# Kernel tuning notes

Hardware: AMD Instinct MI355X
Metric: run time of the kernel (lower is better)

The kernel has to match this reference:

```python
import jax, jax.numpy as jnp
import numpy as np

QLEN, MLEN, CMLEN, BSZ, D_MODEL = 1024, 1024, 512, 2, 1024
N_HEAD, D_HEAD, D_INNER = 16, 64, 4096
KLEN = MLEN + CMLEN + QLEN
LN_EPS = 1e-5


def _layer_norm(x, scale, bias):
    mu = jnp.mean(x, axis=-1, keepdims=True)
    var = jnp.var(x, axis=-1, keepdims=True)
    return (x - mu) * jax.lax.rsqrt(var + LN_EPS) * scale + bias


def _rel_shift(x):
    # x: [qlen, klen, bsz, n_head]  (Transformer-XL relative shift)
    q, k, b, n = x.shape
    x = jnp.concatenate([jnp.zeros((q, 1, b, n), x.dtype), x], axis=1)
    x = x.reshape(k + 1, q, b, n)[1:]
    return x.reshape(q, k, b, n)


def setup_inputs() -> dict:
    key = jax.random.key(0)
    ks = jax.random.split(key, 10)
    s = 0.02
    # causal mask: query i (absolute pos MLEN_TOT+i) cannot attend to key j > MLEN_TOT+i
    mlen_tot = KLEN - QLEN
    i = jnp.arange(QLEN)[:, None]
    j = jnp.arange(KLEN)[None, :]
    attn_mask = j > (i + mlen_tot)
    return {
        "input_ids": jax.random.normal(ks[0], (QLEN, BSZ, D_MODEL), jnp.float32),
        "pos_emb": jax.random.normal(ks[1], (KLEN, D_MODEL), jnp.float32),
        "mem": jax.random.normal(ks[2], (MLEN, BSZ, D_MODEL), jnp.float32),
        "c_mem": jax.random.normal(ks[3], (CMLEN, BSZ, D_MODEL), jnp.float32),
        "attn_mask": attn_mask,
        "qkv_w": jax.random.normal(ks[4], (D_MODEL, 3 * N_HEAD * D_HEAD), jnp.float32) * s,
        "r_w": jax.random.normal(ks[5], (D_MODEL, N_HEAD * D_HEAD), jnp.float32) * s,
        "o_w": jax.random.normal(ks[6], (N_HEAD * D_HEAD, D_MODEL), jnp.float32) * s,
        "r_w_bias": jax.random.normal(ks[7], (N_HEAD, D_HEAD), jnp.float32) * s,
        "r_r_bias": jax.random.normal(ks[8], (N_HEAD, D_HEAD), jnp.float32) * s,
        "ln_attn_scale": jnp.ones((D_MODEL,), jnp.float32),
        "ln_attn_bias": jnp.zeros((D_MODEL,), jnp.float32),
        "ff_w1": jax.random.normal(ks[9], (D_MODEL, D_INNER), jnp.float32) * s,
        "ff_b1": jnp.zeros((D_INNER,), jnp.float32),
        "ff_w2": jax.random.normal(jax.random.fold_in(key, 11), (D_INNER, D_MODEL), jnp.float32) * s,
        "ff_b2": jnp.zeros((D_MODEL,), jnp.float32),
        "ln_ff_scale": jnp.ones((D_MODEL,), jnp.float32),
        "ln_ff_bias": jnp.zeros((D_MODEL,), jnp.float32),
    }


def reference(input_ids, pos_emb, mem, c_mem, attn_mask, qkv_w, r_w, o_w,
              r_w_bias, r_r_bias, ln_attn_scale, ln_attn_bias,
              ff_w1, ff_b1, ff_w2, ff_b2, ln_ff_scale, ln_ff_bias):
    qlen, bsz, d_model = input_ids.shape
    n_head, d_head = r_w_bias.shape
    scale = 1.0 / np.sqrt(d_head)

    # _concat_memories + cat with current sequence (seq-first, dim 0)
    mems = jnp.concatenate([mem, c_mem], axis=0)
    cat = jnp.concatenate([mems, input_ids], axis=0)          # [klen, b, d]

    w_heads = cat @ qkv_w                                     # [klen, b, 3*h*dh]
    w_q, w_k, w_v = jnp.split(w_heads, 3, axis=-1)
    w_q = w_q[-qlen:]
    klen = w_k.shape[0]

    w_q = w_q.reshape(qlen, bsz, n_head, d_head)
    w_k = w_k.reshape(klen, bsz, n_head, d_head)
    w_v = w_v.reshape(klen, bsz, n_head, d_head)
    r_k = (pos_emb @ r_w).reshape(klen, n_head, d_head)       # [klen, h, dh]

    AC = jnp.einsum('ibnd,jbnd->ijbn', w_q + r_w_bias, w_k)
    BD = jnp.einsum('ibnd,jnd->ijbn', w_q + r_r_bias, r_k)
    BD = _rel_shift(BD)
    attn_score = (AC + BD) * scale                            # [q, k, b, h]

    attn_score = jnp.where(attn_mask[:, :, None, None], jnp.float32(-1e30), attn_score)
    attn_prob = jax.nn.softmax(attn_score, axis=1)

    attn_vec = jnp.einsum('ijbn,jbnd->ibnd', attn_prob, w_v)
    attn_vec = attn_vec.reshape(qlen, bsz, n_head * d_head)
    attn_out = attn_vec @ o_w

    # post-lnorm residual (pre_lnorm=False)
    attn_res = _layer_norm(input_ids + attn_out, ln_attn_scale, ln_attn_bias)

    # PositionwiseFF (post-lnorm)
    h = jax.nn.relu(attn_res @ ff_w1 + ff_b1) @ ff_w2 + ff_b2
    out = _layer_norm(attn_res + h, ln_ff_scale, ln_ff_bias)
    return out
```

## Files before the change

kernel.cpp:

```cpp
#include <hip/hip_runtime.h>
#include <hip/hip_bf16.h>

#define QLEN 1024
#define KLEN 2560
#define MTOT 1536
#define BSZ 2
#define NH 16
#define DH 64
#define DMODEL 1024
#define DINNER 4096

typedef short bf16x8 __attribute__((ext_vector_type(8)));
typedef float f32x4  __attribute__((ext_vector_type(4)));

__device__ __forceinline__ short f2bf(float f) {
    union { float f; unsigned u; } v; v.f = f;
    unsigned r = v.u + 0x7FFFu + ((v.u >> 16) & 1u);
    return (short)(r >> 16);
}
__device__ __forceinline__ float bf2f(short s) {
    union { unsigned u; float f; } v; v.u = ((unsigned)(unsigned short)s) << 16;
    return v.f;
}
__device__ __forceinline__ unsigned pack2(float a, float b) {
    unsigned pk;
    asm("v_cvt_pk_bf16_f32 %0, %1, %2" : "=v"(pk) : "v"(a), "v"(b));
    return pk;
}

#define GLOAD16(g, l)                                                        \
    __builtin_amdgcn_global_load_lds(                                        \
        (const __attribute__((address_space(1))) unsigned int*)(g),          \
        (__attribute__((address_space(3))) unsigned int*)(l), 16, 0, 0)

__device__ __forceinline__ void tr_body(
    const float* __restrict__ in, short* __restrict__ out,
    int K, int N, int bx, int by, int tid, float (*ts)[65])
{
    const int k0 = by * 64, n0 = bx * 64;
    const int r = tid >> 2, cb = (tid & 3) * 16;
    #pragma unroll
    for (int u = 0; u < 16; u += 4) {
        const float4 v = *(const float4*)(in + (size_t)(k0 + r) * N + n0 + cb + u);
        ts[r][cb + u] = v.x; ts[r][cb + u + 1] = v.y;
        ts[r][cb + u + 2] = v.z; ts[r][cb + u + 3] = v.w;
    }
    __syncthreads();
    #pragma unroll
    for (int p = 0; p < 4; p++) {
        const int wr_ = (tid >> 4) + p * 16;
        const int c   = (tid & 15) * 4;
        uint2 pk;
        pk.x = pack2(ts[c][wr_], ts[c + 1][wr_]);
        pk.y = pack2(ts[c + 2][wr_], ts[c + 3][wr_]);
        *(uint2*)(out + (size_t)(n0 + wr_) * K + k0 + c) = pk;
    }
}

__global__ __launch_bounds__(256) void prep_all(
    const float* __restrict__ mem, const float* __restrict__ cmem,
    const float* __restrict__ inp, short* __restrict__ catb,
    const float* __restrict__ pos, short* __restrict__ posb,
    const float* __restrict__ qkv_w, short* __restrict__ qkv_wt,
    const float* __restrict__ r_w, short* __restrict__ r_wt,
    const float* __restrict__ o_w, short* __restrict__ o_wt,
    const float* __restrict__ ff_w1, short* __restrict__ ff1t,
    const float* __restrict__ ff_w2, short* __restrict__ ff2t)
{
    __shared__ float ts[64][65];
    const int bid = blockIdx.x;
    const int tid = threadIdx.x;
    if (bid < 2560) {
        const int i = bid * 256 + tid;
        const int row = i >> 7, c = (i & 127) * 8;
        const float* src;
        if (row < 2048)      src = mem  + (size_t)row * 1024;
        else if (row < 3072) src = cmem + (size_t)(row - 2048) * 1024;
        else                 src = inp  + (size_t)(row - 3072) * 1024;
        const float4 a = *(const float4*)(src + c);
        const float4 b = *(const float4*)(src + c + 4);
        uint4 o;
        o.x = pack2(a.x, a.y); o.y = pack2(a.z, a.w);
        o.z = pack2(b.x, b.y); o.w = pack2(b.z, b.w);
        *(uint4*)(catb + (size_t)i * 8) = o;
    } else if (bid < 3840) {
        const int i = (bid - 2560) * 256 + tid;
        const float4 a = *(const float4*)(pos + (size_t)i * 8);
        const float4 b = *(const float4*)(pos + (size_t)i * 8 + 4);
        uint4 o;
        o.x = pack2(a.x, a.y); o.y = pack2(a.z, a.w);
        o.z = pack2(b.x, b.y); o.w = pack2(b.z, b.w);
        *(uint4*)(posb + (size_t)i * 8) = o;
    } else if (bid < 4608) {
        const int r = bid - 3840; tr_body(qkv_w, qkv_wt, 1024, 3072, r % 48, r / 48, tid, ts);
    } else if (bid < 4864) {
        const int r = bid - 4608; tr_body(r_w, r_wt, 1024, 1024, r % 16, r / 16, tid, ts);
    } else if (bid < 5120) {
        const int r = bid - 4864; tr_body(o_w, o_wt, 1024, 1024, r % 16, r / 16, tid, ts);
    } else if (bid < 6144) {
        const int r = bid - 5120; tr_body(ff_w1, ff1t, 1024, 4096, r % 64, r / 64, tid, ts);
    } else {
        const int r = bid - 6144; tr_body(ff_w2, ff2t, 4096, 1024, r % 16, r / 16, tid, ts);
    }
}

__global__ __launch_bounds__(256) void vt_conv(
    const short* __restrict__ wh, short* __restrict__ vt)
{
    __shared__ short Ts[64][72];
    const int j0 = blockIdx.x * 64;
    const int bn = blockIdx.y;
    const int b = bn >> 4, n = bn & 15;
    const int tid = threadIdx.x;
    {
        const int key = tid >> 2, c = (tid & 3) * 16;
        const short* p = wh + ((size_t)(j0 + key) * BSZ + b) * 3072 + 2048 + n * 64 + c;
        *(bf16x8*)&Ts[key][c]     = *(const bf16x8*)p;
        *(bf16x8*)&Ts[key][c + 8] = *(const bf16x8*)(p + 8);
    }
    __syncthreads();
    {
        const int d = tid >> 2, kc = (tid & 3) * 16;
        __attribute__((aligned(16))) short tmp[16];
        #pragma unroll
        for (int u = 0; u < 16; u++) tmp[u] = Ts[kc + u][d];
        short* q = vt + ((size_t)(bn * 64) + d) * KLEN + j0 + kc;
        *(uint4*)q       = *(uint4*)tmp;
        *(uint4*)(q + 8) = *((uint4*)tmp + 1);
    }
}

__device__ __forceinline__ void gemm_core(
    const short* __restrict__ A, const short* __restrict__ Bt,
    short* As, short* Bs, int Kfull, int klen, int bm, int bn,
    int tid, f32x4 acc[4][4])
{
    const int w  = tid >> 6;
    const int l  = tid & 63;
    const int lg = l >> 4, lc = l & 15;
    const int wr = w >> 1, wc = w & 1;
    const int srow = 2 * w * 16 + (l >> 2);
    const int scol = (l & 3) * 8;
    const size_t aoff0 = (size_t)(bm + srow) * Kfull + scol;
    const size_t boff0 = (size_t)(bn + srow) * Kfull + scol;
    const size_t rstep = (size_t)16 * Kfull;
    const int ch0 = 2 * w * 512, ch1 = (2 * w + 1) * 512;

    GLOAD16(A + aoff0, As + ch0);
    GLOAD16(A + aoff0 + rstep, As + ch1);
    GLOAD16(Bt + boff0, Bs + ch0);
    GLOAD16(Bt + boff0 + rstep, Bs + ch1);
    __syncthreads();

    int cur = 0;
    for (int k0 = 0; k0 < klen; k0 += 32) {
        const int nb = (cur ^ 1) * 4096;
        if (k0 + 32 < klen) {
            GLOAD16(A + aoff0 + k0 + 32, As + nb + ch0);
            GLOAD16(A + aoff0 + rstep + k0 + 32, As + nb + ch1);
            GLOAD16(Bt + boff0 + k0 + 32, Bs + nb + ch0);
            GLOAD16(Bt + boff0 + rstep + k0 + 32, Bs + nb + ch1);
        }
        const int cb = cur * 4096;
        bf16x8 af[4], bfr[4];
        #pragma unroll
        for (int m = 0; m < 4; m++)
            af[m] = *(const bf16x8*)(As + cb + (wr * 64 + m * 16 + lc) * 32 + lg * 8);
        #pragma unroll
        for (int n = 0; n < 4; n++)
            bfr[n] = *(const bf16x8*)(Bs + cb + (wc * 64 + n * 16 + lc) * 32 + lg * 8);
        #pragma unroll
        for (int m = 0; m < 4; m++)
            #pragma unroll
            for (int n = 0; n < 4; n++)
                acc[m][n] = __builtin_amdgcn_mfma_f32_16x16x32_bf16(
                    af[m], bfr[n], acc[m][n], 0, 0, 0);
        __syncthreads();
        cur ^= 1;
    }
}

__global__ __launch_bounds__(256) void gemm_g12(
    const short* __restrict__ catb, const short* __restrict__ qkv_wt,
    short* __restrict__ whb,
    const short* __restrict__ posb, const short* __restrict__ r_wt,
    short* __restrict__ rkb)
{
    __shared__ short As[8192], Bs[8192];
    const int tid = threadIdx.x;
    const int id0 = blockIdx.x;
    int id = (id0 & 7) * 116 + (id0 >> 3);
    const short *A, *Bt; short* Cb; int N, bm, bn;
    if (id < 384) {
        A = catb; Bt = qkv_wt; Cb = whb; N = 3072;
        bm = (id >> 4) * 128; bn = (8 + (id & 15)) * 128;
    } else if (id < 768) {
        id -= 384;
        A = catb; Bt = qkv_wt; Cb = whb; N = 3072;
        bm = (24 + id / 24) * 128; bn = (id % 24) * 128;
    } else {
        id -= 768;
        A = posb; Bt = r_wt; Cb = rkb; N = 1024;
        bm = (id / 8) * 128; bn = (id % 8) * 128;
    }

    f32x4 acc[4][4];
    #pragma unroll
    for (int m = 0; m < 4; m++)
        #pragma unroll
        for (int n = 0; n < 4; n++) acc[m][n] = (f32x4){0.f, 0.f, 0.f, 0.f};
    gemm_core(A, Bt, As, Bs, 1024, 1024, bm, bn, tid, acc);

    const int w = tid >> 6, l = tid & 63, lg = l >> 4, lc = l & 15;
    const int wr = w >> 1, wc = w & 1;
    #pragma unroll
    for (int m = 0; m < 4; m++)
        #pragma unroll
        for (int n = 0; n < 4; n++) {
            const int col = bn + wc * 64 + n * 16 + lc;
            #pragma unroll
            for (int r = 0; r < 4; r++) {
                const int row = bm + wr * 64 + m * 16 + lg * 4 + r;
                Cb[(size_t)row * N + col] = f2bf(acc[m][n][r]);
            }
        }
}

__global__ __launch_bounds__(256) void gemm_relu(
    const short* __restrict__ A, const short* __restrict__ Bt,
    const float* __restrict__ bias, short* __restrict__ Cb,
    int N, int K)
{
    __shared__ short As[8192], Bs[8192];
    const int tid = threadIdx.x;
    const int nbx = N >> 7;
    const int lid = blockIdx.x;
    const int nwg8 = gridDim.x >> 3;
    const int swz = (lid & 7) * nwg8 + (lid >> 3);
    const int bn = (swz % nbx) * 128, bm = (swz / nbx) * 128;
    f32x4 acc[4][4];
    #pragma unroll
    for (int m = 0; m < 4; m++)
        #pragma unroll
        for (int n = 0; n < 4; n++) acc[m][n] = (f32x4){0.f, 0.f, 0.f, 0.f};
    gemm_core(A, Bt, As, Bs, K, K, bm, bn, tid, acc);

    const int w = tid >> 6, l = tid & 63, lg = l >> 4, lc = l & 15;
    const int wr = w >> 1, wc = w & 1;
    #pragma unroll
    for (int m = 0; m < 4; m++)
        #pragma unroll
        for (int n = 0; n < 4; n++) {
            const int col = bn + wc * 64 + n * 16 + lc;
            const float bv = bias[col];
            #pragma unroll
            for (int r = 0; r < 4; r++) {
                const int row = bm + wr * 64 + m * 16 + lg * 4 + r;
                Cb[(size_t)row * N + col] = f2bf(fmaxf(acc[m][n][r] + bv, 0.0f));
            }
        }
}

__global__ __launch_bounds__(256) void gemm_split(
    const short* __restrict__ A, const short* __restrict__ Bt,
    float* __restrict__ C0, float* __restrict__ C1,
    int N, int Kfull, int Ksub)
{
    __shared__ short As[8192], Bs[8192];
    const int tid = threadIdx.x;
    const int nbx = N >> 7;
    const int lid = blockIdx.x;
    const int nwg8 = gridDim.x >> 3;
    const int swz = (lid & 7) * nwg8 + (lid >> 3);
    const int bn = (swz % nbx) * 128;
    const int rest = swz / nbx;
    const int bm = (rest & 15) * 128;
    const int z = rest >> 4;
    float* C = z ? C1 : C0;
    f32x4 acc[4][4];
    #pragma unroll
    for (int m = 0; m < 4; m++)
        #pragma unroll
        for (int n = 0; n < 4; n++) acc[m][n] = (f32x4){0.f, 0.f, 0.f, 0.f};
    gemm_core(A + z * Ksub, Bt + z * Ksub, As, Bs, Kfull, Ksub, bm, bn, tid, acc);

    const int w = tid >> 6, l = tid & 63, lg = l >> 4, lc = l & 15;
    const int wr = w >> 1, wc = w & 1;
    #pragma unroll
    for (int m = 0; m < 4; m++)
        #pragma unroll
        for (int n = 0; n < 4; n++) {
            const int col = bn + wc * 64 + n * 16 + lc;
            #pragma unroll
            for (int r = 0; r < 4; r++) {
                const int row = bm + wr * 64 + m * 16 + lg * 4 + r;
                C[(size_t)row * N + col] = acc[m][n][r];
            }
        }
}

__global__ __launch_bounds__(512, 2) void attn_mfma(
    const short* __restrict__ wh,
    const short* __restrict__ vt,
    const short* __restrict__ rk,
    const float* __restrict__ rwb,
    const float* __restrict__ rrb,
    short* __restrict__ po,
    float* __restrict__ ml)
{
    __shared__ __align__(16) short Ks[2][64 * 64];
    __shared__ __align__(16) short Vs[2][64 * 64];
    __shared__ __align__(16) short Rs[256 * 64];
    __shared__ __align__(16) short Ps[8][16 * 64];

    const int bid = blockIdx.x;
    const int ibp = (bid >> 3) & 7;
    const int z   = (bid >> 6) & 1;
    const int bn  = ((bid & 7) << 2) | (bid >> 7);
    const int i0  = ibp * 128;
    const int b   = bn >> 4, n = bn & 15;
    const int tid = threadIdx.x;
    const int w   = tid >> 6;
    const int l   = tid & 63;
    const int lg  = l >> 4;
    const int lc  = l & 15;
    const int i_base = i0 + 16 * w;

    bf16x8 aqw[2], aqr[2];
    {
        const int i = i_base + lc;
        const short* qp = wh + ((size_t)(MTOT + i) * BSZ + b) * 3072 + n * 64;
        #pragma unroll
        for (int kc2 = 0; kc2 < 2; kc2++) {
            const bf16x8 q8 = *(const bf16x8*)(qp + kc2 * 32 + lg * 8);
            const int d0 = kc2 * 32 + lg * 8;
            #pragma unroll
            for (int e = 0; e < 8; e++) {
                const float qv = bf2f(q8[e]);
                aqw[kc2][e] = f2bf(qv + rwb[n * 64 + d0 + e]);
                aqr[kc2][e] = f2bf(qv + rrb[n * 64 + d0 + e]);
            }
        }
    }

    f32x4 o_acc[4];
    #pragma unroll
    for (int nt = 0; nt < 4; nt++) o_acc[nt] = (f32x4){0.f, 0.f, 0.f, 0.f};
    float mrun[4]  = {0.f, 0.f, 0.f, 0.f};
    float lpart[4] = {0.f, 0.f, 0.f, 0.f};

    const int jend   = i0 + 1664;
    const int jhalf  = i0 / 2 + 832;
    const int jstart = z ? jhalf : 0;
    const int jstop  = z ? jend  : jhalf;

    const int kr = tid >> 3, kc = tid & 7;
    const size_t whK = (size_t)b * 3072 + 1024 + n * 64;
    const size_t vtK = (size_t)(bn * 64) * KLEN;
    const int mbase0 = jstart - i0 + 896;

    #pragma unroll
    for (int u = 0; u < 3; u++) {
        const int m = mbase0 + kr + 64 * u;
        bf16x8 rv = (bf16x8){0, 0, 0, 0, 0, 0, 0, 0};
        if (m < KLEN)
            rv = *(const bf16x8*)(rk + (size_t)m * 1024 + n * 64 + kc * 8);
        const int slot = m & 255;
        *(bf16x8*)(Rs + slot * 64 + ((kc ^ (slot & 7)) * 8)) = rv;
    }
    {
        const bf16x8 k0 = *(const bf16x8*)(wh + (size_t)(jstart + kr) * (BSZ * 3072) + whK + kc * 8);
        const bf16x8 v0 = *(const bf16x8*)(vt + vtK + (size_t)kr * KLEN + jstart + kc * 8);
        *(bf16x8*)(Ks[0] + kr * 64 + ((kc ^ (kr & 7)) * 8)) = k0;
        *(bf16x8*)(Vs[0] + kr * 64 + ((kc ^ (kr & 7)) * 8)) = v0;
    }
    bf16x8 pk = (bf16x8){0,0,0,0,0,0,0,0}, pv = pk, pr;
    {
        const int jn = jstart + 64;
        if (jn < jstop) {
            pk = *(const bf16x8*)(wh + (size_t)(jn + kr) * (BSZ * 3072) + whK + kc * 8);
            pv = *(const bf16x8*)(vt + vtK + (size_t)kr * KLEN + jn + kc * 8);
        }
        const int m = mbase0 + 192 + kr;
        pr = (m < KLEN) ? *(const bf16x8*)(rk + (size_t)m * 1024 + n * 64 + kc * 8)
                        : (bf16x8){0, 0, 0, 0, 0, 0, 0, 0};
    }

    int cur = 0;
    for (int j0 = jstart; j0 < jstop; j0 += 64) {
        const int mbase = j0 - i0 + 896;
        __syncthreads();
        *(bf16x8*)(Ks[cur ^ 1] + kr * 64 + ((kc ^ (kr & 7)) * 8)) = pk;
        *(bf16x8*)(Vs[cur ^ 1] + kr * 64 + ((kc ^ (kr & 7)) * 8)) = pv;
        {
            const int mw = mbase + 192 + kr;
            const int slot = mw & 255;
            *(bf16x8*)(Rs + slot * 64 + ((kc ^ (slot & 7)) * 8)) = pr;
        }
        {
            const int jn = j0 + 128;
            if (jn < jstop) {
                pk = *(const bf16x8*)(wh + (size_t)(jn + kr) * (BSZ * 3072) + whK + kc * 8);
                pv = *(const bf16x8*)(vt + vtK + (size_t)kr * KLEN + jn + kc * 8);
            }
            const int m = mbase + 256 + kr;
            pr = (m < KLEN) ? *(const bf16x8*)(rk + (size_t)m * 1024 + n * 64 + kc * 8)
                            : (bf16x8){0, 0, 0, 0, 0, 0, 0, 0};
        }

        __builtin_amdgcn_s_setprio(1);
        f32x4 sfr[4];
        #pragma unroll
        for (int jt = 0; jt < 4; jt++) {
            const int row = 16 * jt + lc;
            const int c0 = (lg ^ (row & 7)) * 8, c1 = ((4 + lg) ^ (row & 7)) * 8;
            const bf16x8 bk0 = *(const bf16x8*)(Ks[cur] + row * 64 + c0);
            const bf16x8 bk1 = *(const bf16x8*)(Ks[cur] + row * 64 + c1);
            f32x4 acc = (f32x4){0.f, 0.f, 0.f, 0.f};
            acc = __builtin_amdgcn_mfma_f32_16x16x32_bf16(aqw[0], bk0, acc, 0, 0, 0);
            acc = __builtin_amdgcn_mfma_f32_16x16x32_bf16(aqw[1], bk1, acc, 0, 0, 0);
            sfr[jt] = acc;
        }
        f32x4 dr[5];
        #pragma unroll
        for (int mt = 0; mt < 5; mt++) {
            const int slot = (mbase + 16 * mt + lc + 112 - 16 * w) & 255;
            const int c0 = (lg ^ (slot & 7)) * 8, c1 = ((4 + lg) ^ (slot & 7)) * 8;
            const bf16x8 br0 = *(const bf16x8*)(Rs + slot * 64 + c0);
            const bf16x8 br1 = *(const bf16x8*)(Rs + slot * 64 + c1);
            f32x4 acc = (f32x4){0.f, 0.f, 0.f, 0.f};
            acc = __builtin_amdgcn_mfma_f32_16x16x32_bf16(aqr[0], br0, acc, 0, 0, 0);
            acc = __builtin_amdgcn_mfma_f32_16x16x32_bf16(aqr[1], br1, acc, 0, 0, 0);
            dr[mt] = acc;
        }
        __builtin_amdgcn_s_setprio(0);

        #pragma unroll
        for (int r = 0; r < 4; r++) {
            const int q   = 4 * lg + r;
            const int o   = lc + 15 - q;
            const int src = (l & 48) | (o & 15);
            float sv[4];
            float mx = -1e30f;
            #pragma unroll
            for (int jt = 0; jt < 4; jt++) {
                const float v0 = __shfl(dr[jt][r], src);
                const float v1 = __shfl(dr[jt + 1][r], src);
                const float bd = (o < 16) ? v0 : v1;
                float s = (sfr[jt][r] + bd) * 0.125f;
                if (z) {
                    const int j = j0 + 16 * jt + lc;
                    if (j > i_base + q + MTOT) s = -1e30f;
                }
                sv[jt] = s;
                mx = fmaxf(mx, s);
            }
            if (__any(mx - mrun[r] > 8.0f)) {
                #pragma unroll
                for (int msk = 1; msk <= 8; msk <<= 1)
                    mx = fmaxf(mx, __shfl_xor(mx, msk));
                const float mnew = fmaxf(mrun[r], mx);
                const float corr = __expf(mrun[r] - mnew);
                mrun[r] = mnew;
                lpart[r] *= corr;
                #pragma unroll
                for (int nt = 0; nt < 4; nt++) o_acc[nt][r] *= corr;
            }
            float p0 = __expf(sv[0] - mrun[r]);
            float p1 = __expf(sv[1] - mrun[r]);
            float p2 = __expf(sv[2] - mrun[r]);
            float p3 = __expf(sv[3] - mrun[r]);
            lpart[r] += (p0 + p1) + (p2 + p3);
            const unsigned pk01 = pack2(p0, p1);
            const unsigned pk23 = pack2(p2, p3);
            short* pw = Ps[w] + q * 64 + (lc & 7);
            const int qs = q & 7;
            pw[(((0 + (lc >> 3)) ^ qs) * 8)] = (short)(pk01 & 0xffffu);
            pw[(((2 + (lc >> 3)) ^ qs) * 8)] = (short)(pk01 >> 16);
            pw[(((4 + (lc >> 3)) ^ qs) * 8)] = (short)(pk23 & 0xffffu);
            pw[(((6 + (lc >> 3)) ^ qs) * 8)] = (short)(pk23 >> 16);
        }

        asm volatile("s_waitcnt lgkmcnt(0)" ::: "memory");
        __builtin_amdgcn_sched_barrier(0);

        __builtin_amdgcn_s_setprio(1);
        const int pc0 = (lg ^ (lc & 7)) * 8, pc1 = ((4 + lg) ^ (lc & 7)) * 8;
        const bf16x8 pa0 = *(const bf16x8*)(Ps[w] + lc * 64 + pc0);
        const bf16x8 pa1 = *(const bf16x8*)(Ps[w] + lc * 64 + pc1);
        #pragma unroll
        for (int nt = 0; nt < 4; nt++) {
            const int row = 16 * nt + lc;
            const int c0 = (lg ^ (row & 7)) * 8, c1 = ((4 + lg) ^ (row & 7)) * 8;
            const bf16x8 bv0 = *(const bf16x8*)(Vs[cur] + row * 64 + c0);
            const bf16x8 bv1 = *(const bf16x8*)(Vs[cur] + row * 64 + c1);
            o_acc[nt] = __builtin_amdgcn_mfma_f32_16x16x32_bf16(pa0, bv0, o_acc[nt], 0, 0, 0);
            o_acc[nt] = __builtin_amdgcn_mfma_f32_16x16x32_bf16(pa1, bv1, o_acc[nt], 0, 0, 0);
        }
        __builtin_amdgcn_s_setprio(0);
        cur ^= 1;
    }

    const size_t blk = (size_t)z * 256 + ibp * 32 + bn;
    #pragma unroll
    for (int r = 0; r < 4; r++) {
        float lr = lpart[r];
        #pragma unroll
        for (int msk = 1; msk <= 8; msk <<= 1)
            lr += __shfl_xor(lr, msk);
        const int q = 16 * w + 4 * lg + r;
        #pragma unroll
        for (int nt = 0; nt < 4; nt++)
            po[(blk * 128 + q) * 64 + 16 * nt + lc] = f2bf(o_acc[nt][r]);
        if (lc == 0) {
            ml[(blk * 128 + q) * 2 + 0] = mrun[r];
            ml[(blk * 128 + q) * 2 + 1] = lr;
        }
    }
}

__global__ __launch_bounds__(256) void attn_merge(
    const short* __restrict__ po, const float* __restrict__ ml,
    short* __restrict__ av)
{
    const int blk = blockIdx.x;
    const int ib2 = blk >> 5, bn = blk & 31;
    const int b = bn >> 4, n = bn & 15;
    const int tid = threadIdx.x;
    const int q64 = tid >> 2, dc = (tid & 3) * 16;
    const int i = ib2 * 64 + q64;
    const size_t r0 = ((size_t)(i >> 7) * 32 + bn) * 128 + (i & 127);
    const size_t r1 = ((size_t)(256 + (i >> 7) * 32 + bn)) * 128 + (i & 127);
    const float m0 = ml[r0 * 2], l0 = ml[r0 * 2 + 1];
    const float m1 = ml[r1 * 2], l1 = ml[r1 * 2 + 1];
    const float M = fmaxf(m0, m1);
    const float c0 = __expf(m0 - M), c1 = __expf(m1 - M);
    const float invL = 1.0f / (l0 * c0 + l1 * c1);
    const bf16x8 a0 = *(const bf16x8*)(po + r0 * 64 + dc);
    const bf16x8 a1 = *(const bf16x8*)(po + r0 * 64 + dc + 8);
    const bf16x8 b0 = *(const bf16x8*)(po + r1 * 64 + dc);
    const bf16x8 b1 = *(const bf16x8*)(po + r1 * 64 + dc + 8);
    __attribute__((aligned(16))) short ov[16];
    #pragma unroll
    for (int e = 0; e < 8; e++) {
        ov[e]     = f2bf((bf2f(a0[e]) * c0 + bf2f(b0[e]) * c1) * invL);
        ov[e + 8] = f2bf((bf2f(a1[e]) * c0 + bf2f(b1[e]) * c1) * invL);
    }
    short* op = av + ((size_t)i * BSZ + b) * 1024 + n * 64 + dc;
    *(uint4*)op       = *(uint4*)ov;
    *(uint4*)(op + 8) = *((uint4*)ov + 1);
}

template <bool WB, bool HASB>
__global__ __launch_bounds__(256) void ln_fuse(
    const float* __restrict__ p0, const float* __restrict__ p1,
    const float* __restrict__ badd, const float* __restrict__ res,
    const float* __restrict__ scale, const float* __restrict__ bias,
    float* __restrict__ out, short* __restrict__ outb)
{
    const int row = blockIdx.x;
    const int tid = threadIdx.x;
    const size_t base = (size_t)row * 1024 + tid * 4;
    const float4 a = *(const float4*)(p0 + base);
    const float4 b = *(const float4*)(p1 + base);
    const float4 rv = *(const float4*)(res + base);
    float v[4] = {a.x + b.x + rv.x, a.y + b.y + rv.y,
                  a.z + b.z + rv.z, a.w + b.w + rv.w};
    if (HASB) {
        const float4 bb = *(const float4*)(badd + tid * 4);
        v[0] += bb.x; v[1] += bb.y; v[2] += bb.z; v[3] += bb.w;
    }
    float s  = v[0] + v[1] + v[2] + v[3];
    float ss = v[0]*v[0] + v[1]*v[1] + v[2]*v[2] + v[3]*v[3];
    #pragma unroll
    for (int off = 32; off >= 1; off >>= 1) {
        s  += __shfl_down(s, off);
        ss += __shfl_down(ss, off);
    }
    __shared__ float red[8];
    const int lane = tid & 63, wid = tid >> 6;
    if (lane == 0) { red[wid] = s; red[4 + wid] = ss; }
    __syncthreads();
    if (tid == 0) {
        red[0] = red[0] + red[1] + red[2] + red[3];
        red[4] = red[4] + red[5] + red[6] + red[7];
    }
    __syncthreads();
    const float mean = red[0] * (1.0f / 1024.0f);
    const float var  = red[4] * (1.0f / 1024.0f) - mean * mean;
    const float rstd = rsqrtf(var + 1e-5f);
    const float4 sc = *(const float4*)(scale + tid * 4);
    const float4 bi = *(const float4*)(bias + tid * 4);
    float4 o;
    o.x = (v[0] - mean) * rstd * sc.x + bi.x;
    o.y = (v[1] - mean) * rstd * sc.y + bi.y;
    o.z = (v[2] - mean) * rstd * sc.z + bi.z;
    o.w = (v[3] - mean) * rstd * sc.w + bi.w;
    *(float4*)(out + base) = o;
    if (WB) {
        uint2 pk;
        pk.x = pack2(o.x, o.y);
        pk.y = pack2(o.z, o.w);
        *(uint2*)(outb + base) = pk;
    }
}

extern "C" void kernel_launch(void* const* d_in, const int* in_sizes, int n_in,
                              void* d_out, int out_size, void* d_ws, size_t ws_size,
                              hipStream_t stream) {
    const float* input_ids = (const float*)d_in[0];
    const float* pos_emb   = (const float*)d_in[1];
    const float* mem       = (const float*)d_in[2];
    const float* c_mem     = (const float*)d_in[3];
    const float* qkv_w     = (const float*)d_in[5];
    const float* r_w       = (const float*)d_in[6];
    const float* o_w       = (const float*)d_in[7];
    const float* r_w_bias  = (const float*)d_in[8];
    const float* r_r_bias  = (const float*)d_in[9];
    const float* ln_a_s    = (const float*)d_in[10];
    const float* ln_a_b    = (const float*)d_in[11];
    const float* ff_w1     = (const float*)d_in[12];
    const float* ff_b1     = (const float*)d_in[13];
    const float* ff_w2     = (const float*)d_in[14];
    const float* ff_b2     = (const float*)d_in[15];
    const float* ln_f_s    = (const float*)d_in[16];
    const float* ln_f_b    = (const float*)d_in[17];

    char* base = (char*)d_ws;
    short* o_wt   = (short*)(base + 0);
    short* ff1t   = (short*)(base + 2097152);
    short* ff2t   = (short*)(base + 10485760);
    short* whb    = (short*)(base + 18874368);
    short* rkb    = (short*)(base + 50331648);
    short* qkv_wt = (short*)(base + 55574528);
    short* catb   = (short*)(base + 61865984);
    short* posb   = (short*)(base + 72351744);
    short* r_wt   = (short*)(base + 77594624);
    short* vtb    = (short*)(base + 55574528);
    short* po     = (short*)(base + 66060288);
    float* mlb    = (float*)(base + 74448896);
    short* avb    = (short*)(base + 74973184);
    float* hp0    = (float*)(base + 18874368);
    float* hp1    = (float*)(base + 27262976);
    float* ares   = (float*)(base + 35651584);
    short* aresb  = (short*)(base + 44040192);
    short* h1b    = (short*)(base + 48234496);

    const dim3 thr(256);

    prep_all<<<dim3(7168), thr, 0, stream>>>(
        mem, c_mem, input_ids, catb, pos_emb, posb,
        qkv_w, qkv_wt, r_w, r_wt, o_w, o_wt, ff_w1, ff1t, ff_w2, ff2t);
    gemm_g12<<<dim3(928), thr, 0, stream>>>(catb, qkv_wt, whb, posb, r_wt, rkb);
    vt_conv<<<dim3(40, 32), thr, 0, stream>>>(whb, vtb);
    attn_mfma<<<dim3(512), dim3(512), 0, stream>>>(
        whb, vtb, rkb, r_w_bias, r_r_bias, po, mlb);
    attn_merge<<<dim3(512), thr, 0, stream>>>(po, mlb, avb);
    gemm_split<<<dim3(256), thr, 0, stream>>>(
        avb, o_wt, hp0, hp1, 1024, 1024, 512);
    ln_fuse<true, false><<<dim3(2048), thr, 0, stream>>>(
        hp0, hp1, nullptr, input_ids, ln_a_s, ln_a_b, ares, aresb);
    gemm_relu<<<dim3(512), thr, 0, stream>>>(aresb, ff1t, ff_b1, h1b, 4096, 1024);
    gemm_split<<<dim3(256), thr, 0, stream>>>(
        h1b, ff2t, hp0, hp1, 1024, 4096, 2048);
    ln_fuse<false, true><<<dim3(2048), thr, 0, stream>>>(
        hp0, hp1, ff_b2, ares, ln_f_s, ln_f_b, (float*)d_out, nullptr);
}
```

Before: 249.7 us.

## Triple-buffer GEMM LDS with single barrier and read bf16 residual in final LN

The shared GEMM core moves from double to triple buffering of LDS tiles. Global loads are issued two k-steps ahead, and each iteration uses an explicit vmcnt wait plus one barrier instead of two __syncthreads. Separately, the first layernorm no longer writes an fp32 copy of its output, and the second layernorm reads the bf16 residual instead. This saves memory traffic but introduces an extra bf16 rounding of the residual. LDS per block grows from 32KB to 48KB, which may lower occupancy.

Measured after the change: 263.9 us. +5.7%, slower.

```diff
diff --git a/kernel.cpp b/kernel.cpp
--- a/kernel.cpp
+++ b/kernel.cpp
@@ -150,33 +150,41 @@
     GLOAD16(A + aoff0 + rstep, As + ch1);
     GLOAD16(Bt + boff0, Bs + ch0);
     GLOAD16(Bt + boff0 + rstep, Bs + ch1);
-    __syncthreads();
-
-    int cur = 0;
+    if (32 < klen) {
+        GLOAD16(A + aoff0 + 32, As + 4096 + ch0);
+        GLOAD16(A + aoff0 + rstep + 32, As + 4096 + ch1);
+        GLOAD16(Bt + boff0 + 32, Bs + 4096 + ch0);
+        GLOAD16(Bt + boff0 + rstep + 32, Bs + 4096 + ch1);
+    }
+
+    int bufr = 0;
     for (int k0 = 0; k0 < klen; k0 += 32) {
-        const int nb = (cur ^ 1) * 4096;
-        if (k0 + 32 < klen) {
-            GLOAD16(A + aoff0 + k0 + 32, As + nb + ch0);
-            GLOAD16(A + aoff0 + rstep + k0 + 32, As + nb + ch1);
-            GLOAD16(Bt + boff0 + k0 + 32, Bs + nb + ch0);
-            GLOAD16(Bt + boff0 + rstep + k0 + 32, Bs + nb + ch1);
-        }
-        const int cb = cur * 4096;
-        bf16x8 af[4], bfr[4];
+        if (k0 + 32 < klen) asm volatile("s_waitcnt vmcnt(4)" ::: "memory");
+        else                asm volatile("s_waitcnt vmcnt(0)" ::: "memory");
+        __builtin_amdgcn_s_barrier();
+        __builtin_amdgcn_sched_barrier(0);
+        if (k0 + 64 < klen) {
+            const int nb = ((bufr + 2) >= 3 ? bufr - 1 : bufr + 2) * 4096;
+            GLOAD16(A + aoff0 + k0 + 64, As + nb + ch0);
+            GLOAD16(A + aoff0 + rstep + k0 + 64, As + nb + ch1);
+            GLOAD16(Bt + boff0 + k0 + 64, Bs + nb + ch0);
+            GLOAD16(Bt + boff0 + rstep + k0 + 64, Bs + nb + ch1);
+        }
+        const int cb = bufr * 4096;
+        bf16x8 af[4], bfr_[4];
         #pragma unroll
         for (int m = 0; m < 4; m++)
             af[m] = *(const bf16x8*)(As + cb + (wr * 64 + m * 16 + lc) * 32 + lg * 8);
         #pragma unroll
         for (int n = 0; n < 4; n++)
-            bfr[n] = *(const bf16x8*)(Bs + cb + (wc * 64 + n * 16 + lc) * 32 + lg * 8);
+            bfr_[n] = *(const bf16x8*)(Bs + cb + (wc * 64 + n * 16 + lc) * 32 + lg * 8);
         #pragma unroll
         for (int m = 0; m < 4; m++)
             #pragma unroll
             for (int n = 0; n < 4; n++)
                 acc[m][n] = __builtin_amdgcn_mfma_f32_16x16x32_bf16(
-                    af[m], bfr[n], acc[m][n], 0, 0, 0);
-        __syncthreads();
-        cur ^= 1;
+                    af[m], bfr_[n], acc[m][n], 0, 0, 0);
+        bufr = (bufr + 1 == 3) ? 0 : bufr + 1;
     }
 }
 
@@ -186,7 +194,7 @@
     const short* __restrict__ posb, const short* __restrict__ r_wt,
     short* __restrict__ rkb)
 {
-    __shared__ short As[8192], Bs[8192];
+    __shared__ short As[12288], Bs[12288];
     const int tid = threadIdx.x;
     const int id0 = blockIdx.x;
     int id = (id0 & 7) * 116 + (id0 >> 3);
@@ -231,7 +239,7 @@
     const float* __restrict__ bias, short* __restrict__ Cb,
     int N, int K)
 {
-    __shared__ short As[8192], Bs[8192];
+    __shared__ short As[12288], Bs[12288];
     const int tid = threadIdx.x;
     const int nbx = N >> 7;
     const int lid = blockIdx.x;
@@ -266,7 +274,7 @@
     float* __restrict__ C0, float* __restrict__ C1,
     int N, int Kfull, int Ksub)
 {
-    __shared__ short As[8192], Bs[8192];
+    __shared__ short As[12288], Bs[12288];
     const int tid = threadIdx.x;
     const int nbx = N >> 7;
     const int lid = blockIdx.x;
@@ -551,21 +559,32 @@
     *(uint4*)(op + 8) = *((uint4*)ov + 1);
 }
 
-template <bool WB, bool HASB>
+template <int OUTBF, bool HASB, bool RESB>
 __global__ __launch_bounds__(256) void ln_fuse(
     const float* __restrict__ p0, const float* __restrict__ p1,
-    const float* __restrict__ badd, const float* __restrict__ res,
+    const float* __restrict__ badd,
+    const float* __restrict__ resf, const short* __restrict__ resb,
     const float* __restrict__ scale, const float* __restrict__ bias,
-    float* __restrict__ out, short* __restrict__ outb)
+    float* __restrict__ outf, short* __restrict__ outb)
 {
     const int row = blockIdx.x;
     const int tid = threadIdx.x;
     const size_t base = (size_t)row * 1024 + tid * 4;
     const float4 a = *(const float4*)(p0 + base);
     const float4 b = *(const float4*)(p1 + base);
-    const float4 rv = *(const float4*)(res + base);
-    float v[4] = {a.x + b.x + rv.x, a.y + b.y + rv.y,
-                  a.z + b.z + rv.z, a.w + b.w + rv.w};
+    float rv[4];
+    if (RESB) {
+        const uint2 rr = *(const uint2*)(resb + base);
+        rv[0] = bf2f((short)(rr.x & 0xffffu));
+        rv[1] = bf2f((short)(rr.x >> 16));
+        rv[2] = bf2f((short)(rr.y & 0xffffu));
+        rv[3] = bf2f((short)(rr.y >> 16));
+    } else {
+        const float4 rf = *(const float4*)(resf + base);
+        rv[0] = rf.x; rv[1] = rf.y; rv[2] = rf.z; rv[3] = rf.w;
+    }
+    float v[4] = {a.x + b.x + rv[0], a.y + b.y + rv[1],
+                  a.z + b.z + rv[2], a.w + b.w + rv[3]};
     if (HASB) {
         const float4 bb = *(const float4*)(badd + tid * 4);
         v[0] += bb.x; v[1] += bb.y; v[2] += bb.z; v[3] += bb.w;
@@ -591,17 +610,17 @@
     const float rstd = rsqrtf(var + 1e-5f);
     const float4 sc = *(const float4*)(scale + tid * 4);
     const float4 bi = *(const float4*)(bias + tid * 4);
-    float4 o;
-    o.x = (v[0] - mean) * rstd * sc.x + bi.x;
-    o.y = (v[1] - mean) * rstd * sc.y + bi.y;
-    o.z = (v[2] - mean) * rstd * sc.z + bi.z;
-    o.w = (v[3] - mean) * rstd * sc.w + bi.w;
-    *(float4*)(out + base) = o;
-    if (WB) {
+    float o0 = (v[0] - mean) * rstd * sc.x + bi.x;
+    float o1 = (v[1] - mean) * rstd * sc.y + bi.y;
+    float o2 = (v[2] - mean) * rstd * sc.z + bi.z;
+    float o3 = (v[3] - mean) * rstd * sc.w + bi.w;
+    if (OUTBF) {
         uint2 pk;
-        pk.x = pack2(o.x, o.y);
-        pk.y = pack2(o.z, o.w);
+        pk.x = pack2(o0, o1);
+        pk.y = pack2(o2, o3);
         *(uint2*)(outb + base) = pk;
+    } else {
+        *(float4*)(outf + base) = make_float4(o0, o1, o2, o3);
     }
 }
 
@@ -642,7 +661,6 @@
     short* avb    = (short*)(base + 74973184);
     float* hp0    = (float*)(base + 18874368);
     float* hp1    = (float*)(base + 27262976);
-    float* ares   = (float*)(base + 35651584);
     short* aresb  = (short*)(base + 44040192);
     short* h1b    = (short*)(base + 48234496);
 
@@ -658,11 +676,11 @@
     attn_merge<<<dim3(512), thr, 0, stream>>>(po, mlb, avb);
     gemm_split<<<dim3(256), thr, 0, stream>>>(
         avb, o_wt, hp0, hp1, 1024, 1024, 512);
-    ln_fuse<true, false><<<dim3(2048), thr, 0, stream>>>(
-        hp0, hp1, nullptr, input_ids, ln_a_s, ln_a_b, ares, aresb);
+    ln_fuse<1, false, false><<<dim3(2048), thr, 0, stream>>>(
+        hp0, hp1, nullptr, input_ids, nullptr, ln_a_s, ln_a_b, nullptr, aresb);
     gemm_relu<<<dim3(512), thr, 0, stream>>>(aresb, ff1t, ff_b1, h1b, 4096, 1024);
     gemm_split<<<dim3(256), thr, 0, stream>>>(
         h1b, ff2t, hp0, hp1, 1024, 4096, 2048);
-    ln_fuse<false, true><<<dim3(2048), thr, 0, stream>>>(
-        hp0, hp1, ff_b2, ares, ln_f_s, ln_f_b, (float*)d_out, nullptr);
-}
+    ln_fuse<0, true, true><<<dim3(2048), thr, 0, stream>>>(
+        hp0, hp1, ff_b2, nullptr, aresb, ln_f_s, ln_f_b, (float*)d_out, nullptr);
+}
```
